# Kernel optimization log

Measured on AMD Instinct MI355X. Metric: run time of the kernel, lower is better.

## Reference

```python
import jax, jax.numpy as jnp
import numpy as np

C = 768        # n_embd
HSZ = 64       # HEAD_SIZE (module-level global in source)
H = C // HSZ   # n_head = 12
G = 2          # conv groups
DL = HSZ       # D_MIX_LORA = HEAD_SIZE
DD = 64        # TIME_DECAY_DIM
DG = C // 4    # D_GATE_LORA
B, T = 2, 2048

PNAMES = ['time_maa_x','time_maa_r','time_maa_w','time_maa_k','time_maa_v','time_maa_a','time_maa_g',
          'time_decay','time_faaaa','time_aaaaa','maa_w1','maa_w2','decay_w1','decay_w2','aaa_w1','aaa_w2',
          'kkk_w1','kkk_w2','gate_w1','gate_w2','w_key','w_value','w_receptance','w_output','ln_x_weight']

def setup_inputs() -> dict:
    key = jax.random.key(0)
    ks = jax.random.split(key, 32)
    f = lambda i, shape, s=1.0: jax.random.normal(ks[i], shape, jnp.float32) * s
    u = lambda i, shape: jax.random.uniform(ks[i], shape, dtype=jnp.float32)
    cs = float(C // G) ** -0.5
    return dict(
        x=f(0, (B, C, T)),
        time_maa_x=u(1, (1, C, 1)), time_maa_r=u(2, (1, C, 1)), time_maa_w=u(3, (1, C, 1)),
        time_maa_k=u(4, (1, C, 1)), time_maa_v=u(5, (1, C, 1)), time_maa_a=u(6, (1, C, 1)),
        time_maa_g=u(7, (1, C, 1)),
        time_decay=f(8, (1, C, 1), 0.5), time_faaaa=f(9, (H, HSZ), 0.1), time_aaaaa=f(10, (1, C, 1), 0.1),
        maa_w1=f(11, (6 * DL, C), 0.02), maa_w2=f(12, (6, DL, C), 0.02),
        decay_w1=f(13, (DD, C), 0.02), decay_w2=f(14, (C, DD), 0.02),
        aaa_w1=f(15, (DD, C), 0.02), aaa_w2=f(16, (C, DD), 0.02),
        kkk_w1=f(17, (DD, C), 0.02), kkk_w2=f(18, (C, DD), 0.02),
        gate_w1=f(19, (DG, C), 0.02), gate_w2=f(20, (C, DG), 0.02),
        w_key=f(21, (G, C // G, C // G), cs), w_value=f(22, (G, C // G, C // G), cs),
        w_receptance=f(23, (G, C // G, C // G), cs), w_output=f(24, (G, C // G, C // G), cs),
        ln_x_weight=jnp.ones((C,), jnp.float32),
    )

def _gconv(x, w):
    # grouped 1x1 Conv1d: x (B,C,T), w (G, C/G out, C/G in) -> (B,C,T)
    b, c, t = x.shape
    xg = x.reshape(b, G, c // G, t)
    return jnp.einsum('goc,bgct->bgot', w, xg).reshape(b, c, t)

def _lora(w1, w2, z):
    # w2 @ tanh(w1 @ z), channels-first z (B,C,T)
    return jnp.einsum('cd,bdt->bct', w2, jnp.tanh(jnp.einsum('dc,bct->bdt', w1, z)))

def _wkv7(r, w, k, v, a, bb):
    # RWKV-7 generalized delta-rule recurrence. All inputs (B,T,C), w in log-decay space.
    b, t, c = r.shape
    rs = lambda x: jnp.moveaxis(x.reshape(b, t, H, HSZ), 1, 0)  # (T,B,H,N)
    r4, k4, v4, a4, b4 = map(rs, (r, k, v, a, bb))
    wdec = rs(jnp.exp(-jnp.exp(w)))
    def step(S, inp):
        rr, ww, kk, vv, aa, b2 = inp  # each (B,H,N)
        sab = jnp.einsum('bhij,bhj,bhk->bhik', S, aa, b2)
        S = S * ww[:, :, None, :] + sab + vv[..., None] * kk[:, :, None, :]
        y = jnp.einsum('bhij,bhj->bhi', S, rr)
        return S, y
    S0 = jnp.zeros((b, H, HSZ, HSZ), r.dtype)
    _, ys = jax.lax.scan(step, S0, (r4, wdec, k4, v4, a4, b4))
    return jnp.moveaxis(ys, 0, 1).reshape(b, t, c)

def _forward(x, time_maa_x, time_maa_r, time_maa_w, time_maa_k, time_maa_v, time_maa_a, time_maa_g,
             time_decay, time_faaaa, time_aaaaa, maa_w1, maa_w2, decay_w1, decay_w2, aaa_w1, aaa_w2,
             kkk_w1, kkk_w2, gate_w1, gate_w2, w_key, w_value, w_receptance, w_output, ln_x_weight):
    b, c, t = x.shape
    xx = x  # shift_mode == 'none'
    xm = x * time_maa_x + xx * (1.0 - time_maa_x)
    tm = jnp.tanh(jnp.einsum('dc,bct->bdt', maa_w1, xm)).reshape(b, 6, DL, t)
    mix = jnp.einsum('bndt,ndc->nbct', tm, maa_w2)  # (6,B,C,T)
    mr, mw, mk, mv, ma, mg = mix
    xr = x + xx * (time_maa_r + mr)
    xw = x + xx * (time_maa_w + mw)
    xk = x + xx * (time_maa_k + mk)
    xv = x + xx * (time_maa_v + mv)
    xa = x + xx * (time_maa_a + ma)
    xg = x + xx * (time_maa_g + mg)
    tr = lambda z: z.transpose(0, 2, 1)  # (B,C,T) -> (B,T,C)
    r = tr(_gconv(xr, w_receptance))
    wlog = tr(-jax.nn.softplus(-(time_decay + _lora(decay_w1, decay_w2, xw))) - 0.5)
    k = tr(_gconv(xk, w_key))
    v = tr(_gconv(xv, w_value))
    g = tr(_lora(gate_w1, gate_w2, xg))
    kk = k + tr(_lora(kkk_w1, kkk_w2, xk))
    kk4 = kk.reshape(b, t, H, HSZ)
    kk = (kk4 / jnp.maximum(jnp.linalg.norm(kk4, axis=-1, keepdims=True), 1e-12)).reshape(b, t, c)
    a = jax.nn.sigmoid(tr(time_aaaaa + _lora(aaa_w1, aaa_w2, xa)))
    y = _wkv7(r, wlog, k, v, -kk, kk * a)
    # ln_x: RMSNorm over channel dim
    y = y * jax.lax.rsqrt(jnp.mean(y * y, axis=-1, keepdims=True) + 1e-5) * ln_x_weight
    rk = (r.reshape(b, t, H, HSZ) * k.reshape(b, t, H, HSZ) * time_faaaa).sum(-1, keepdims=True)
    y = y + (rk * v.reshape(b, t, H, HSZ)).reshape(b, t, c)
    return _gconv(tr(y * g), w_output)  # (B,C,T)

def reference(x, time_maa_x, time_maa_r, time_maa_w, time_maa_k, time_maa_v, time_maa_a, time_maa_g,
              time_decay, time_faaaa, time_aaaaa, maa_w1, maa_w2, decay_w1, decay_w2, aaa_w1, aaa_w2,
              kkk_w1, kkk_w2, gate_w1, gate_w2, w_key, w_value, w_receptance, w_output, ln_x_weight):
    return _forward(x, time_maa_x, time_maa_r, time_maa_w, time_maa_k, time_maa_v, time_maa_a, time_maa_g,
                    time_decay, time_faaaa, time_aaaaa, maa_w1, maa_w2, decay_w1, decay_w2, aaa_w1, aaa_w2,
                    kkk_w1, kkk_w2, gate_w1, gate_w2, w_key, w_value, w_receptance, w_output, ln_x_weight)
```

## Files before the change

### kernel.cpp

```cpp
#include <hip/hip_runtime.h>
#include <math.h>

#define BB 2
#define TT 2048
#define CC 768
#define HH 12
#define NN 64
#define GG 2
#define CG 384
#define FF 3145728L
#define S1 1572864L

typedef __attribute__((ext_vector_type(8))) short bf8frag;
typedef __attribute__((ext_vector_type(4))) float f4acc;

__device__ inline unsigned short f2bf(float x) {
    union { float f; unsigned u; } v; v.f = x;
    unsigned r = v.u + 0x7FFFu + ((v.u >> 16) & 1u);
    return (unsigned short)(r >> 16);
}
__device__ inline float bf2f(unsigned short u) {
    union { unsigned u; float f; } v; v.u = ((unsigned)u) << 16;
    return v.f;
}

template<int ATRANS, int BTRANS, int TOUT, int MODE>
__global__ __launch_bounds__(256) void gemm_kernel(
    const float* __restrict__ A, const float* __restrict__ Bm, float* __restrict__ Cm,
    const float* __restrict__ aux, const float* __restrict__ aux2,
    int K, int ldA, int ldB, int ldC, int zInner,
    long sA_o, long sA_i, long sB_o, long sB_i, long sC_o, long sC_i,
    long sAux_i, long sAux2_o, unsigned short* bfout)
{
    const int zo = blockIdx.z / zInner;
    const int zi = blockIdx.z % zInner;
    A  += (size_t)zo * sA_o + (size_t)zi * sA_i;
    Bm += (size_t)zo * sB_o + (size_t)zi * sB_i;
    Cm += (size_t)zo * sC_o + (size_t)zi * sC_i;
    if (MODE == 2) { aux += (size_t)zi * sAux_i; aux2 += (size_t)zo * sAux2_o; }

    const int m0t = blockIdx.y * 64;
    const int n0t = blockIdx.x * 64;
    const int tid = threadIdx.x;

    __shared__ float As[16][64];
    __shared__ float Bs[16][64];

    int mi, ni;
    if (TOUT) { mi = (tid & 15) * 4; ni = (tid >> 4) * 4; }
    else      { ni = (tid & 15) * 4; mi = (tid >> 4) * 4; }

    float acc[4][4];
#pragma unroll
    for (int i = 0; i < 4; ++i)
#pragma unroll
        for (int j = 0; j < 4; ++j) acc[i][j] = 0.f;

    for (int k0 = 0; k0 < K; k0 += 16) {
        if (!ATRANS) {
            const int row = tid >> 2;
            const int kc  = (tid & 3) * 4;
            float4 av = *(const float4*)&A[(size_t)(m0t + row) * ldA + k0 + kc];
            As[kc + 0][row] = av.x; As[kc + 1][row] = av.y;
            As[kc + 2][row] = av.z; As[kc + 3][row] = av.w;
        } else {
            const int krow = tid >> 4;
            const int mc   = (tid & 15) * 4;
            *(float4*)&As[krow][mc] = *(const float4*)&A[(size_t)(k0 + krow) * ldA + m0t + mc];
        }
        if (!BTRANS) {
            const int krow = tid >> 4;
            const int tc   = (tid & 15) * 4;
            *(float4*)&Bs[krow][tc] = *(const float4*)&Bm[(size_t)(k0 + krow) * ldB + n0t + tc];
        } else {
            const int trow = tid >> 2;
            const int kc   = (tid & 3) * 4;
            float4 bv = *(const float4*)&Bm[(size_t)(n0t + trow) * ldB + k0 + kc];
            Bs[kc + 0][trow] = bv.x; Bs[kc + 1][trow] = bv.y;
            Bs[kc + 2][trow] = bv.z; Bs[kc + 3][trow] = bv.w;
        }
        __syncthreads();
#pragma unroll
        for (int kk = 0; kk < 16; ++kk) {
            float4 a4 = *(const float4*)&As[kk][mi];
            float4 b4 = *(const float4*)&Bs[kk][ni];
            float am[4] = {a4.x, a4.y, a4.z, a4.w};
            float bn[4] = {b4.x, b4.y, b4.z, b4.w};
#pragma unroll
            for (int i = 0; i < 4; ++i)
#pragma unroll
                for (int j = 0; j < 4; ++j) acc[i][j] = fmaf(am[i], bn[j], acc[i][j]);
        }
        __syncthreads();
    }

    const int mbase = m0t + mi, nbase = n0t + ni;
#pragma unroll
    for (int i = 0; i < 4; ++i) {
        float4 xv;
        if (MODE == 2) xv = *(const float4*)&aux2[(size_t)(mbase + i) * ldC + nbase];
        float xa[4] = {0.f, 0.f, 0.f, 0.f};
        if (MODE == 2) { xa[0] = xv.x; xa[1] = xv.y; xa[2] = xv.z; xa[3] = xv.w; }
#pragma unroll
        for (int j = 0; j < 4; ++j) {
            float v = acc[i][j];
            if (MODE == 1) v = tanhf(v);
            else if (MODE == 2) v = xa[j] * (aux[mbase + i] + v);
            else if (MODE == 3) {
                float u  = aux[mbase + i] + v;
                float sp = fmaxf(-u, 0.f) + log1pf(expf(-fabsf(u)));
                float wl = -sp - 0.5f;
                v = expf(-expf(wl));
            } else if (MODE == 4) {
                float u = aux[mbase + i] + v;
                v = 1.f / (1.f + expf(-u));
            }
            acc[i][j] = v;
        }
    }
    if (!TOUT) {
        const bool skipf = (MODE == 2) && (bfout != nullptr) && (zi == 0 || zi == 3);
        if (!skipf) {
#pragma unroll
            for (int i = 0; i < 4; ++i) {
                float4 o = {acc[i][0], acc[i][1], acc[i][2], acc[i][3]};
                *(float4*)&Cm[(size_t)(mbase + i) * ldC + nbase] = o;
            }
        }
        if (MODE == 2 && bfout != nullptr) {
            int sidx = (zi == 0) ? 0 : (zi == 2) ? 1 : (zi == 3) ? 2 : -1;
            if (sidx >= 0) {
                unsigned short* bp = bfout + (size_t)sidx * FF + (size_t)zo * ((long)CC * TT);
#pragma unroll
                for (int i = 0; i < 4; ++i) {
                    ushort4 o = {f2bf(acc[i][0]), f2bf(acc[i][1]), f2bf(acc[i][2]), f2bf(acc[i][3])};
                    *(ushort4*)&bp[(size_t)(mbase + i) * ldC + nbase] = o;
                }
            }
        }
    } else {
#pragma unroll
        for (int j = 0; j < 4; ++j) {
            float4 o = {acc[0][j], acc[1][j], acc[2][j], acc[3][j]};
            *(float4*)&Cm[(size_t)(nbase + j) * ldC + mbase] = o;
        }
    }
}

__global__ __launch_bounds__(256) void lorah_kernel(
    const float* __restrict__ w0, const float* __restrict__ w1,
    const float* __restrict__ w2, const float* __restrict__ w3,
    const float* __restrict__ x0, const float* __restrict__ x1,
    const float* __restrict__ x2, const float* __restrict__ x3,
    float* __restrict__ o0, float* __restrict__ o1,
    float* __restrict__ o2, float* __restrict__ o3)
{
    const int z = blockIdx.z;
    const int which = z >> 1, bz = z & 1;
    if (which < 3 && blockIdx.y > 0) return;
    const float* A; const float* Bm; float* Cm; int M;
    if (which == 0)      { A = w0; Bm = x0; Cm = o0; M = 64; }
    else if (which == 1) { A = w1; Bm = x1; Cm = o1; M = 64; }
    else if (which == 2) { A = w2; Bm = x2; Cm = o2; M = 64; }
    else                 { A = w3; Bm = x3; Cm = o3; M = 192; }
    Bm += (size_t)bz * ((long)CC * TT);
    Cm += (size_t)bz * ((long)M * TT);

    const int m0t = blockIdx.y * 64;
    const int n0t = blockIdx.x * 64;
    const int tid = threadIdx.x;

    __shared__ float As[16][64];
    __shared__ float Bs[16][64];

    const int ni = (tid & 15) * 4, mi = (tid >> 4) * 4;
    float acc[4][4];
#pragma unroll
    for (int i = 0; i < 4; ++i)
#pragma unroll
        for (int j = 0; j < 4; ++j) acc[i][j] = 0.f;

    for (int k0 = 0; k0 < CC; k0 += 16) {
        {
            const int row = tid >> 2, kc = (tid & 3) * 4;
            float4 av = *(const float4*)&A[(size_t)(m0t + row) * CC + k0 + kc];
            As[kc + 0][row] = av.x; As[kc + 1][row] = av.y;
            As[kc + 2][row] = av.z; As[kc + 3][row] = av.w;
        }
        {
            const int krow = tid >> 4, tc = (tid & 15) * 4;
            *(float4*)&Bs[krow][tc] = *(const float4*)&Bm[(size_t)(k0 + krow) * TT + n0t + tc];
        }
        __syncthreads();
#pragma unroll
        for (int kk = 0; kk < 16; ++kk) {
            float4 a4 = *(const float4*)&As[kk][mi];
            float4 b4 = *(const float4*)&Bs[kk][ni];
            float am[4] = {a4.x, a4.y, a4.z, a4.w};
            float bn[4] = {b4.x, b4.y, b4.z, b4.w};
#pragma unroll
            for (int i = 0; i < 4; ++i)
#pragma unroll
                for (int j = 0; j < 4; ++j) acc[i][j] = fmaf(am[i], bn[j], acc[i][j]);
        }
        __syncthreads();
    }
    const int mbase = m0t + mi, nbase = n0t + ni;
#pragma unroll
    for (int i = 0; i < 4; ++i) {
        float4 o = {tanhf(acc[i][0]), tanhf(acc[i][1]), tanhf(acc[i][2]), tanhf(acc[i][3])};
        *(float4*)&Cm[(size_t)(mbase + i) * TT + nbase] = o;
    }
}

__global__ __launch_bounds__(256) void loraout_kernel(
    const float* __restrict__ dw2, const float* __restrict__ aw2,
    const float* __restrict__ kw2,
    const float* __restrict__ dhh, const float* __restrict__ ahh,
    const float* __restrict__ khh,
    const float* __restrict__ tdecay, const float* __restrict__ taaaaa,
    float* __restrict__ wwB, float* __restrict__ b2B, float* __restrict__ aaB)
{
    const int z = blockIdx.z;
    const int which = z >> 1, bz = z & 1;
    const float* A; const float* Bm; float* Cm; const float* aux;
    if (which == 0)      { A = dw2; Bm = dhh; Cm = wwB; aux = tdecay; }
    else if (which == 1) { A = aw2; Bm = ahh; Cm = b2B; aux = taaaaa; }
    else                 { A = kw2; Bm = khh; Cm = aaB; aux = nullptr; }
    Bm += (size_t)bz * (64L * TT);
    Cm += (size_t)bz * ((long)TT * CC);

    const int m0t = blockIdx.y * 64;
    const int n0t = blockIdx.x * 64;
    const int tid = threadIdx.x;

    __shared__ float As[16][64];
    __shared__ float Bs[16][64];

    const int mi = (tid & 15) * 4, ni = (tid >> 4) * 4;
    float acc[4][4];
#pragma unroll
    for (int i = 0; i < 4; ++i)
#pragma unroll
        for (int j = 0; j < 4; ++j) acc[i][j] = 0.f;

    for (int k0 = 0; k0 < 64; k0 += 16) {
        {
            const int row = tid >> 2, kc = (tid & 3) * 4;
            float4 av = *(const float4*)&A[(size_t)(m0t + row) * 64 + k0 + kc];
            As[kc + 0][row] = av.x; As[kc + 1][row] = av.y;
            As[kc + 2][row] = av.z; As[kc + 3][row] = av.w;
        }
        {
            const int krow = tid >> 4, tc = (tid & 15) * 4;
            *(float4*)&Bs[krow][tc] = *(const float4*)&Bm[(size_t)(k0 + krow) * TT + n0t + tc];
        }
        __syncthreads();
#pragma unroll
        for (int kk = 0; kk < 16; ++kk) {
            float4 a4 = *(const float4*)&As[kk][mi];
            float4 b4 = *(const float4*)&Bs[kk][ni];
            float am[4] = {a4.x, a4.y, a4.z, a4.w};
            float bn[4] = {b4.x, b4.y, b4.z, b4.w};
#pragma unroll
            for (int i = 0; i < 4; ++i)
#pragma unroll
                for (int j = 0; j < 4; ++j) acc[i][j] = fmaf(am[i], bn[j], acc[i][j]);
        }
        __syncthreads();
    }
    const int mbase = m0t + mi, nbase = n0t + ni;
#pragma unroll
    for (int i = 0; i < 4; ++i) {
#pragma unroll
        for (int j = 0; j < 4; ++j) {
            float v = acc[i][j];
            if (which == 0) {
                float u  = aux[mbase + i] + v;
                float sp = fmaxf(-u, 0.f) + log1pf(expf(-fabsf(u)));
                v = expf(-expf(-sp - 0.5f));
            } else if (which == 1) {
                float u = aux[mbase + i] + v;
                v = 1.f / (1.f + expf(-u));
            }
            acc[i][j] = v;
        }
    }
#pragma unroll
    for (int j = 0; j < 4; ++j) {
        float4 o = {acc[0][j], acc[1][j], acc[2][j], acc[3][j]};
        *(float4*)&Cm[(size_t)(nbase + j) * CC + mbase] = o;
    }
}

__global__ __launch_bounds__(256) void convs3_mfma_kernel(
    const unsigned short* __restrict__ wball, const unsigned short* __restrict__ X6t,
    float* __restrict__ X6)
{
    const int z = blockIdx.z;
    const int conv = z >> 2, bg = z & 3, b = bg >> 1, g = bg & 1;
    const unsigned short* Wb = wball + (size_t)conv * 294912;
    const unsigned short* Xb = X6t + (size_t)conv * FF;
    const int oslot = (conv == 0) ? 1 : (conv == 1) ? 4 : 5;
    float* Cout = X6 + (size_t)oslot * FF;

    const int t0 = blockIdx.x * 128;
    const int m0 = blockIdx.y * 128;
    const int tid = threadIdx.x;
    const int wave = tid >> 6, lane = tid & 63;
    const int lq = lane >> 4, lr = lane & 15;

    __shared__ unsigned short Ws[128 * 40];
    __shared__ unsigned short Xs[128 * 40];

    const unsigned short* Wg = Wb + (size_t)g * (CG * CG);
    const long xbase = (long)b * (long)TT * CC;

    f4acc acc0[8], acc1[8];
#pragma unroll
    for (int j = 0; j < 8; ++j) { acc0[j] = (f4acc)0.f; acc1[j] = (f4acc)0.f; }

    for (int k0 = 0; k0 < CG; k0 += 32) {
        {
            const int m = tid >> 1, kc = (tid & 1) * 16;
            const unsigned short* src = Wg + (size_t)(m0 + m) * CG + k0 + kc;
            *(bf8frag*)&Ws[m * 40 + kc]     = *(const bf8frag*)src;
            *(bf8frag*)&Ws[m * 40 + kc + 8] = *(const bf8frag*)(src + 8);
        }
        {
            const int t = tid >> 1, kc = (tid & 1) * 16;
            const unsigned short* src = Xb + xbase + (long)(t0 + t) * CC + g * CG + k0 + kc;
            *(bf8frag*)&Xs[t * 40 + kc]     = *(const bf8frag*)src;
            *(bf8frag*)&Xs[t * 40 + kc + 8] = *(const bf8frag*)(src + 8);
        }
        __syncthreads();

        bf8frag a0 = *(const bf8frag*)&Ws[(32 * wave + lr) * 40 + lq * 8];
        bf8frag a1 = *(const bf8frag*)&Ws[(32 * wave + 16 + lr) * 40 + lq * 8];
#pragma unroll
        for (int nj = 0; nj < 8; ++nj) {
            bf8frag bb = *(const bf8frag*)&Xs[(16 * nj + lr) * 40 + lq * 8];
            acc0[nj] = __builtin_amdgcn_mfma_f32_16x16x32_bf16(a0, bb, acc0[nj], 0, 0, 0);
            acc1[nj] = __builtin_amdgcn_mfma_f32_16x16x32_bf16(a1, bb, acc1[nj], 0, 0, 0);
        }
        __syncthreads();
    }

#pragma unroll
    for (int fi = 0; fi < 2; ++fi) {
        const int cbase = m0 + 32 * wave + 16 * fi + lq * 4;
#pragma unroll
        for (int nj = 0; nj < 8; ++nj) {
            const f4acc av = fi ? acc1[nj] : acc0[nj];
            const int t = t0 + 16 * nj + lr;
            float4 o = {av[0], av[1], av[2], av[3]};
            *(float4*)&Cout[(long)b * (long)TT * CC + (long)t * CC + g * CG + cbase] = o;
        }
    }
}

__global__ __launch_bounds__(256) void convout_mfma_kernel(
    const unsigned short* __restrict__ Wb, const unsigned short* __restrict__ Xb,
    float* __restrict__ Cout)
{
    const int bz = blockIdx.z; const int b = bz >> 1, g = bz & 1;
    const int t0 = blockIdx.x * 128;
    const int m0 = blockIdx.y * 128;
    const int tid = threadIdx.x;
    const int wave = tid >> 6, lane = tid & 63;
    const int lq = lane >> 4, lr = lane & 15;

    __shared__ unsigned short Ws[128 * 40];
    __shared__ unsigned short Xs[128 * 40];

    const unsigned short* Wg = Wb + (size_t)g * (CG * CG);
    const long xbase = (long)b * (long)TT * CC;

    f4acc acc0[8], acc1[8];
#pragma unroll
    for (int j = 0; j < 8; ++j) { acc0[j] = (f4acc)0.f; acc1[j] = (f4acc)0.f; }

    for (int k0 = 0; k0 < CG; k0 += 32) {
        {
            const int m = tid >> 1, kc = (tid & 1) * 16;
            const unsigned short* src = Wg + (size_t)(m0 + m) * CG + k0 + kc;
            *(bf8frag*)&Ws[m * 40 + kc]     = *(const bf8frag*)src;
            *(bf8frag*)&Ws[m * 40 + kc + 8] = *(const bf8frag*)(src + 8);
        }
        {
            const int t = tid >> 1, kc = (tid & 1) * 16;
            const unsigned short* src = Xb + xbase + (long)(t0 + t) * CC + g * CG + k0 + kc;
            *(bf8frag*)&Xs[t * 40 + kc]     = *(const bf8frag*)src;
            *(bf8frag*)&Xs[t * 40 + kc + 8] = *(const bf8frag*)(src + 8);
        }
        __syncthreads();

        bf8frag a0 = *(const bf8frag*)&Ws[(32 * wave + lr) * 40 + lq * 8];
        bf8frag a1 = *(const bf8frag*)&Ws[(32 * wave + 16 + lr) * 40 + lq * 8];
#pragma unroll
        for (int nj = 0; nj < 8; ++nj) {
            bf8frag bb = *(const bf8frag*)&Xs[(16 * nj + lr) * 40 + lq * 8];
            acc0[nj] = __builtin_amdgcn_mfma_f32_16x16x32_bf16(a0, bb, acc0[nj], 0, 0, 0);
            acc1[nj] = __builtin_amdgcn_mfma_f32_16x16x32_bf16(a1, bb, acc1[nj], 0, 0, 0);
        }
        __syncthreads();
    }

#pragma unroll
    for (int fi = 0; fi < 2; ++fi) {
        const int cbase = m0 + 32 * wave + 16 * fi + lq * 4;
#pragma unroll
        for (int nj = 0; nj < 8; ++nj) {
            const f4acc av = fi ? acc1[nj] : acc0[nj];
            const int t = t0 + 16 * nj + lr;
#pragma unroll
            for (int i = 0; i < 4; ++i)
                Cout[(long)b * (long)CC * TT + (long)(g * CG + cbase + i) * TT + t] = av[i];
        }
    }
}

__global__ __launch_bounds__(256) void maaw1_mfma_kernel(
    const unsigned short* __restrict__ Wb, const unsigned short* __restrict__ Xb,
    float* __restrict__ Cout)
{
    const int b = blockIdx.z;
    const int t0 = blockIdx.x * 128;
    const int m0 = blockIdx.y * 128;
    const int tid = threadIdx.x;
    const int wave = tid >> 6, lane = tid & 63;
    const int lq = lane >> 4, lr = lane & 15;

    __shared__ unsigned short Ws[128 * 40];
    __shared__ unsigned short Xs[128 * 40];

    const long xbase = (long)b * (long)TT * CC;

    f4acc acc0[8], acc1[8];
#pragma unroll
    for (int j = 0; j < 8; ++j) { acc0[j] = (f4acc)0.f; acc1[j] = (f4acc)0.f; }

    for (int k0 = 0; k0 < CC; k0 += 32) {
        {
            const int m = tid >> 1, kc = (tid & 1) * 16;
            const unsigned short* src = Wb + (size_t)(m0 + m) * CC + k0 + kc;
            *(bf8frag*)&Ws[m * 40 + kc]     = *(const bf8frag*)src;
            *(bf8frag*)&Ws[m * 40 + kc + 8] = *(const bf8frag*)(src + 8);
        }
        {
            const int t = tid >> 1, kc = (tid & 1) * 16;
            const unsigned short* src = Xb + xbase + (long)(t0 + t) * CC + k0 + kc;
            *(bf8frag*)&Xs[t * 40 + kc]     = *(const bf8frag*)src;
            *(bf8frag*)&Xs[t * 40 + kc + 8] = *(const bf8frag*)(src + 8);
        }
        __syncthreads();

        bf8frag a0 = *(const bf8frag*)&Ws[(32 * wave + lr) * 40 + lq * 8];
        bf8frag a1 = *(const bf8frag*)&Ws[(32 * wave + 16 + lr) * 40 + lq * 8];
#pragma unroll
        for (int nj = 0; nj < 8; ++nj) {
            bf8frag bb = *(const bf8frag*)&Xs[(16 * nj + lr) * 40 + lq * 8];
            acc0[nj] = __builtin_amdgcn_mfma_f32_16x16x32_bf16(a0, bb, acc0[nj], 0, 0, 0);
            acc1[nj] = __builtin_amdgcn_mfma_f32_16x16x32_bf16(a1, bb, acc1[nj], 0, 0, 0);
        }
        __syncthreads();
    }

#pragma unroll
    for (int fi = 0; fi < 2; ++fi) {
        const int m = m0 + 32 * wave + 16 * fi + lq * 4;
#pragma unroll
        for (int nj = 0; nj < 8; ++nj) {
            const f4acc av = fi ? acc1[nj] : acc0[nj];
            const int t = t0 + 16 * nj + lr;
#pragma unroll
            for (int i = 0; i < 4; ++i)
                Cout[(long)b * 384 * TT + (long)(m + i) * TT + t] = tanhf(av[i]);
        }
    }
}

__global__ __launch_bounds__(256) void btr_kernel(const unsigned short* __restrict__ xin,
                                                  unsigned short* __restrict__ xout)
{
    __shared__ unsigned short L[64][68];
    const int t0 = blockIdx.x * 64, c0 = blockIdx.y * 64;
    const int s = blockIdx.z >> 1, b = blockIdx.z & 1;
    const int tid = threadIdx.x;
    const int lr = tid >> 4, lc = (tid & 15) * 4;
    const size_t ibase = (size_t)s * FF + (size_t)b * CC * TT;
    const size_t obase = (size_t)s * FF + (size_t)b * TT * CC;
#pragma unroll
    for (int i = 0; i < 4; ++i) {
        int c = lr + i * 16;
        ushort4 v = *(const ushort4*)&xin[ibase + (size_t)(c0 + c) * TT + t0 + lc];
        L[c][lc + 0] = v.x; L[c][lc + 1] = v.y; L[c][lc + 2] = v.z; L[c][lc + 3] = v.w;
    }
    __syncthreads();
#pragma unroll
    for (int i = 0; i < 4; ++i) {
        int t = lr + i * 16;
        ushort4 o = {L[lc + 0][t], L[lc + 1][t], L[lc + 2][t], L[lc + 3][t]};
        *(ushort4*)&xout[obase + (size_t)(t0 + t) * CC + c0 + lc] = o;
    }
}

__global__ __launch_bounds__(256) void wcvt_kernel(
    const float* __restrict__ w0, const float* __restrict__ w1,
    const float* __restrict__ w2, const float* __restrict__ w3,
    const float* __restrict__ w4, unsigned short* __restrict__ wb,
    const float* __restrict__ pr, const float* __restrict__ pw,
    const float* __restrict__ pk, const float* __restrict__ pv,
    const float* __restrict__ pa, const float* __restrict__ pg,
    float* __restrict__ paux,
    const float* __restrict__ xin, unsigned short* __restrict__ xout)
{
    __shared__ unsigned short L[64][68];
    const int bid = blockIdx.x;
    if (bid < 5760) {
        const int i = bid * 256 + threadIdx.x;
        const int which = i / 294912, r = i - which * 294912;
        const float* s = (which == 0) ? w0 : (which == 1) ? w1 : (which == 2) ? w2
                       : (which == 3) ? w3 : w4;
        wb[i] = f2bf(s[r]);
        return;
    }
    if (bid < 6528) {
        const int gb = bid - 5760;
        const int t0 = (gb & 31) * 64;
        const int rest = gb >> 5;
        const int c0 = (rest % 12) * 64;
        const int b  = rest / 12;
        const int tid = threadIdx.x;
        const int lr = tid >> 4, lc = (tid & 15) * 4;
#pragma unroll
        for (int i = 0; i < 4; ++i) {
            int c = lr + i * 16;
            float4 v = *(const float4*)&xin[(size_t)b * CC * TT + (size_t)(c0 + c) * TT + t0 + lc];
            L[c][lc + 0] = f2bf(v.x); L[c][lc + 1] = f2bf(v.y);
            L[c][lc + 2] = f2bf(v.z); L[c][lc + 3] = f2bf(v.w);
        }
        __syncthreads();
#pragma unroll
        for (int i = 0; i < 4; ++i) {
            int t = lr + i * 16;
            ushort4 o = {L[lc + 0][t], L[lc + 1][t], L[lc + 2][t], L[lc + 3][t]};
            *(ushort4*)&xout[(size_t)b * TT * CC + (size_t)(t0 + t) * CC + c0 + lc] = o;
        }
        return;
    }
#pragma unroll
    for (int ch = 0; ch < 3; ++ch) {
        int c = ch * 256 + threadIdx.x;
        paux[0 * CC + c] = 1.f + pr[c];
        paux[1 * CC + c] = 1.f + pw[c];
        paux[2 * CC + c] = 1.f + pk[c];
        paux[3 * CC + c] = 1.f + pv[c];
        paux[4 * CC + c] = 1.f + pa[c];
        paux[5 * CC + c] = 1.f + pg[c];
    }
}

__global__ __launch_bounds__(256) void e1_kernel(const float* __restrict__ kA,
                                                 float* __restrict__ kvecA,
                                                 float* __restrict__ aA)
{
    const size_t base = (size_t)blockIdx.x * CC;
    const int tid = threadIdx.x;
#pragma unroll
    for (int ch = 0; ch < 3; ++ch) {
        int c = ch * 256 + tid;
        float kk = kA[base + c] + kvecA[base + c];
        float ss = kk * kk;
#pragma unroll
        for (int off = 32; off; off >>= 1) ss += __shfl_xor(ss, off, 64);
        float denom = fmaxf(sqrtf(ss), 1e-12f);
        float kkn = kk / denom;
        float av = aA[base + c];
        kvecA[base + c] = -kkn;
        aA[base + c]    = kkn * av;
    }
}

struct WFrag {
    float4 w[2], a[2], b[2], k[2], r[2];
    float vv;
};

__global__ __launch_bounds__(256) void wkv_gate_kernel(
    const float* __restrict__ rA, const float* __restrict__ wA,
    const float* __restrict__ kA, const float* __restrict__ vA,
    const float* __restrict__ aaA, const float* __restrict__ b2A,
    unsigned short* __restrict__ yp8,
    const float* __restrict__ gw2, const float* __restrict__ ghh,
    float* __restrict__ gbuf)
{
    if (blockIdx.x < 192) {
        if (threadIdx.x >= 64) return;
        const int blk = blockIdx.x;
        const int bh = blk % 24, rg = blk / 24;
        const int b = bh / HH, h = bh - b * HH;
        const int lane = threadIdx.x;
        const int jg = lane >> 3, p = lane & 7;
        const int row = rg * 8 + p;
        const int base = b * TT * CC + h * NN;
        const int fo = jg * 8;
        const int ybase = (jg * BB + b) * (TT * CC) + h * NN + row;

        float S[8];
#pragma unroll
        for (int i = 0; i < 8; ++i) S[i] = 0.f;

        WFrag f0, f1, f2;

        auto loadfrag = [&](WFrag& f, int t) {
            const int o = base + t * CC + fo;
#pragma unroll
            for (int q = 0; q < 2; ++q) {
                f.w[q] = *(const float4*)&wA[o + 4 * q];
                f.a[q] = *(const float4*)&aaA[o + 4 * q];
                f.b[q] = *(const float4*)&b2A[o + 4 * q];
                f.k[q] = *(const float4*)&kA[o + 4 * q];
                f.r[q] = *(const float4*)&rA[o + 4 * q];
            }
            f.vv = vA[base + t * CC + row];
        };

        auto stepf = [&](const WFrag& f, int t) {
            const float vv = f.vv;
            float vk[8];
#pragma unroll
            for (int q = 0; q < 2; ++q) {
                vk[4*q+0] = vv * f.k[q].x;
                vk[4*q+1] = vv * f.k[q].y;
                vk[4*q+2] = vv * f.k[q].z;
                vk[4*q+3] = vv * f.k[q].w;
            }

            float t0 = 0.f, t1 = 0.f, t2 = 0.f, t3 = 0.f;
#pragma unroll
            for (int q = 0; q < 2; ++q) {
                float4 a4 = f.a[q];
                t0 = fmaf(S[4*q+0], a4.x, t0);
                t1 = fmaf(S[4*q+1], a4.y, t1);
                t2 = fmaf(S[4*q+2], a4.z, t2);
                t3 = fmaf(S[4*q+3], a4.w, t3);
            }
            float part = (t0 + t1) + (t2 + t3);
            float s08 = __shfl_xor(part,  8, 64);
            float s16 = __shfl_xor(part, 16, 64);
            float s24 = __shfl_xor(part, 24, 64);
            float s32 = __shfl_xor(part, 32, 64);
            float s40 = __shfl_xor(part, 40, 64);
            float s48 = __shfl_xor(part, 48, 64);
            float s56 = __shfl_xor(part, 56, 64);
            float tmp = ((part + s08) + (s16 + s24)) + ((s32 + s40) + (s48 + s56));

            float y0 = 0.f, y1 = 0.f, y2 = 0.f, y3 = 0.f;
#pragma unroll
            for (int q = 0; q < 2; ++q) {
                float4 w4 = f.w[q], b4 = f.b[q], r4 = f.r[q];
                S[4*q+0] = fmaf(S[4*q+0], w4.x, fmaf(tmp, b4.x, vk[4*q+0]));
                y0 = fmaf(S[4*q+0], r4.x, y0);
                S[4*q+1] = fmaf(S[4*q+1], w4.y, fmaf(tmp, b4.y, vk[4*q+1]));
                y1 = fmaf(S[4*q+1], r4.y, y1);
                S[4*q+2] = fmaf(S[4*q+2], w4.z, fmaf(tmp, b4.z, vk[4*q+2]));
                y2 = fmaf(S[4*q+2], r4.z, y2);
                S[4*q+3] = fmaf(S[4*q+3], w4.w, fmaf(tmp, b4.w, vk[4*q+3]));
                y3 = fmaf(S[4*q+3], r4.w, y3);
            }
            yp8[ybase + t * CC] = f2bf((y0 + y1) + (y2 + y3));
        };

        loadfrag(f0, 0);
        loadfrag(f1, 1);
        loadfrag(f2, 2);

        int t = 0;
        for (; t + 2 < TT; t += 3) {
            stepf(f0, t);
            if (t + 3 < TT) loadfrag(f0, t + 3);
            stepf(f1, t + 1);
            if (t + 4 < TT) loadfrag(f1, t + 4);
            stepf(f2, t + 2);
            if (t + 5 < TT) loadfrag(f2, t + 5);
        }
        if (t < TT) stepf(f0, t);
        if (t + 1 < TT) stepf(f1, t + 1);
        return;
    }

    {
        const int gb = blockIdx.x - 192;
        const int n0t = (gb & 31) * 64;
        const int rest = gb >> 5;
        const int m0t = (rest % 12) * 64;
        const int bz  = rest / 12;
        const float* A  = gw2;
        const float* Bm = ghh + (size_t)bz * (192L * TT);
        float* Cm = gbuf + (size_t)bz * ((long)TT * CC);
        const int tid = threadIdx.x;

        __shared__ float As[16][64];
        __shared__ float Bs[16][64];

        const int mi = (tid & 15) * 4, ni = (tid >> 4) * 4;
        float acc[4][4];
#pragma unroll
        for (int i = 0; i < 4; ++i)
#pragma unroll
            for (int j = 0; j < 4; ++j) acc[i][j] = 0.f;

        for (int k0 = 0; k0 < 192; k0 += 16) {
            {
                const int row = tid >> 2, kc = (tid & 3) * 4;
                float4 av = *(const float4*)&A[(size_t)(m0t + row) * 192 + k0 + kc];
                As[kc + 0][row] = av.x; As[kc + 1][row] = av.y;
                As[kc + 2][row] = av.z; As[kc + 3][row] = av.w;
            }
            {
                const int krow = tid >> 4, tc = (tid & 15) * 4;
                *(float4*)&Bs[krow][tc] = *(const float4*)&Bm[(size_t)(k0 + krow) * TT + n0t + tc];
            }
            __syncthreads();
#pragma unroll
            for (int kk = 0; kk < 16; ++kk) {
                float4 a4 = *(const float4*)&As[kk][mi];
                float4 b4 = *(const float4*)&Bs[kk][ni];
                float am[4] = {a4.x, a4.y, a4.z, a4.w};
                float bn[4] = {b4.x, b4.y, b4.z, b4.w};
#pragma unroll
                for (int i = 0; i < 4; ++i)
#pragma unroll
                    for (int j = 0; j < 4; ++j) acc[i][j] = fmaf(am[i], bn[j], acc[i][j]);
            }
            __syncthreads();
        }
        const int mbase = m0t + mi, nbase = n0t + ni;
#pragma unroll
        for (int j = 0; j < 4; ++j) {
            float4 o = {acc[0][j], acc[1][j], acc[2][j], acc[3][j]};
            *(float4*)&Cm[(size_t)(nbase + j) * CC + mbase] = o;
        }
    }
}

__global__ __launch_bounds__(256) void e2_kernel(
    const unsigned short* __restrict__ yp8, const float* __restrict__ rA,
    const float* __restrict__ kA, const float* __restrict__ vA,
    const float* __restrict__ gA, const float* __restrict__ faaaa,
    const float* __restrict__ lnw, unsigned short* __restrict__ zB)
{
    const int bt = blockIdx.x;
    const int b = bt / TT, t = bt - b * TT;
    const size_t base = (size_t)bt * CC;
    const int tid = threadIdx.x;
    const int wave = tid >> 6;
    __shared__ float red[4];
    __shared__ float rk[12];

    float yv[3];
    float ss = 0.f;
#pragma unroll
    for (int ch = 0; ch < 3; ++ch) {
        int c = ch * 256 + tid;
        float y = 0.f;
#pragma unroll
        for (int jg = 0; jg < 8; ++jg)
            y += bf2f(yp8[((size_t)(jg * BB + b) * TT + t) * CC + c]);
        yv[ch] = y;
        ss = fmaf(y, y, ss);
        float p = rA[base + c] * kA[base + c] * faaaa[c];
#pragma unroll
        for (int off = 32; off; off >>= 1) p += __shfl_xor(p, off, 64);
        if ((tid & 63) == 0) rk[ch * 4 + wave] = p;
    }
#pragma unroll
    for (int off = 32; off; off >>= 1) ss += __shfl_xor(ss, off, 64);
    if ((tid & 63) == 0) red[wave] = ss;
    __syncthreads();
    const float total = red[0] + red[1] + red[2] + red[3];
    const float scale = rsqrtf(total / (float)CC + 1e-5f);
#pragma unroll
    for (int ch = 0; ch < 3; ++ch) {
        int c = ch * 256 + tid;
        float out = yv[ch] * scale * lnw[c] + rk[c >> 6] * vA[base + c];
        zB[base + c] = f2bf(out * gA[base + c]);
    }
}

extern "C" void kernel_launch(void* const* d_in, const int* in_sizes, int n_in,
                              void* d_out, int out_size, void* d_ws, size_t ws_size,
                              hipStream_t stream)
{
    (void)in_sizes; (void)n_in; (void)out_size; (void)ws_size;
    const float* x        = (const float*)d_in[0];
    const float* tmaa_r   = (const float*)d_in[2];
    const float* tmaa_w   = (const float*)d_in[3];
    const float* tmaa_k   = (const float*)d_in[4];
    const float* tmaa_v   = (const float*)d_in[5];
    const float* tmaa_a   = (const float*)d_in[6];
    const float* tmaa_g   = (const float*)d_in[7];
    const float* tdecay   = (const float*)d_in[8];
    const float* tfaaaa   = (const float*)d_in[9];
    const float* taaaaa   = (const float*)d_in[10];
    const float* maa_w1   = (const float*)d_in[11];
    const float* maa_w2   = (const float*)d_in[12];
    const float* decay_w1 = (const float*)d_in[13];
    const float* decay_w2 = (const float*)d_in[14];
    const float* aaa_w1   = (const float*)d_in[15];
    const float* aaa_w2   = (const float*)d_in[16];
    const float* kkk_w1   = (const float*)d_in[17];
    const float* kkk_w2   = (const float*)d_in[18];
    const float* gate_w1  = (const float*)d_in[19];
    const float* gate_w2  = (const float*)d_in[20];
    const float* w_key    = (const float*)d_in[21];
    const float* w_value  = (const float*)d_in[22];
    const float* w_recept = (const float*)d_in[23];
    const float* w_output = (const float*)d_in[24];
    const float* lnw      = (const float*)d_in[25];
    float* out = (float*)d_out;

    float* ws   = (float*)d_ws;
    float* paux = ws;
    float* tm   = ws + 8192;
    float* X6   = tm + S1;
    float* dh   = X6 + 6 * FF;
    float* ah   = dh + 262144;
    float* kh   = ah + 262144;
    float* gh   = kh + 262144;
    float* gbuf = gh + 786432;
    unsigned short* yp8 = (unsigned short*)(gbuf + FF);
    unsigned short* X6b = yp8 + 8 * FF;
    unsigned short* zb  = X6b + 3 * FF;
    unsigned short* wb  = zb + FF;
    unsigned short* xtb = wb + 5L * 294912;
    unsigned short* X6t = xtb + FF;

    float* xw = X6 + 1 * FF; float* xk = X6 + 2 * FF;
    float* xa = X6 + 4 * FF; float* xg = X6 + 5 * FF;
    float* wwB = X6 + 0 * FF; float* rB  = X6 + 1 * FF; float* aaB = X6 + 2 * FF;
    float* b2B = X6 + 3 * FF; float* kB  = X6 + 4 * FF; float* vB  = X6 + 5 * FF;

    const long CT = (long)CC * TT;
    const long TC = (long)TT * CC;

    wcvt_kernel<<<dim3(6529), 256, 0, stream>>>(
        w_recept, w_key, w_value, w_output, maa_w1, wb,
        tmaa_r, tmaa_w, tmaa_k, tmaa_v, tmaa_a, tmaa_g, paux,
        x, xtb);

    maaw1_mfma_kernel<<<dim3(16, 3, 2), 256, 0, stream>>>(wb + 4L * 294912, xtb, tm);

    gemm_kernel<1,0,0,2><<<dim3(32, 12, 12), 256, 0, stream>>>(
        maa_w2, tm, X6, paux, x,
        64, 768, TT, TT, 6,
        0, 64L * 768, 384L * TT, 64L * TT, CT, FF, 768, CT, X6b);

    btr_kernel<<<dim3(32, 12, 6), 256, 0, stream>>>(X6b, X6t);

    lorah_kernel<<<dim3(32, 3, 8), 256, 0, stream>>>(
        decay_w1, aaa_w1, kkk_w1, gate_w1, xw, xa, xk, xg, dh, ah, kh, gh);

    convs3_mfma_kernel<<<dim3(16, 3, 12), 256, 0, stream>>>(wb, X6t, X6);

    loraout_kernel<<<dim3(32, 12, 6), 256, 0, stream>>>(
        decay_w2, aaa_w2, kkk_w2, dh, ah, kh, tdecay, taaaaa, wwB, b2B, aaB);

    e1_kernel<<<dim3(BB * TT), 256, 0, stream>>>(kB, aaB, b2B);

    wkv_gate_kernel<<<dim3(960), 256, 0, stream>>>(
        rB, wwB, kB, vB, aaB, b2B, yp8, gate_w2, gh, gbuf);

    e2_kernel<<<dim3(BB * TT), 256, 0, stream>>>(yp8, rB, kB, vB, gbuf, tfaaaa, lnw, zb);

    convout_mfma_kernel<<<dim3(16, 3, 4), 256, 0, stream>>>(wb + 3L * 294912, zb, out);
}
```

Baseline: 768.0 us.

## Merge independent lora, transpose and conv kernels into two combined launches

```diff
diff --git a/kernel.cpp b/kernel.cpp
--- a/kernel.cpp
+++ b/kernel.cpp
@@ -147,163 +147,268 @@
     }
 }
 
-__global__ __launch_bounds__(256) void lorah_kernel(
-    const float* __restrict__ w0, const float* __restrict__ w1,
-    const float* __restrict__ w2, const float* __restrict__ w3,
-    const float* __restrict__ x0, const float* __restrict__ x1,
-    const float* __restrict__ x2, const float* __restrict__ x3,
-    float* __restrict__ o0, float* __restrict__ o1,
-    float* __restrict__ o2, float* __restrict__ o3)
-{
-    const int z = blockIdx.z;
-    const int which = z >> 1, bz = z & 1;
-    if (which < 3 && blockIdx.y > 0) return;
-    const float* A; const float* Bm; float* Cm; int M;
-    if (which == 0)      { A = w0; Bm = x0; Cm = o0; M = 64; }
-    else if (which == 1) { A = w1; Bm = x1; Cm = o1; M = 64; }
-    else if (which == 2) { A = w2; Bm = x2; Cm = o2; M = 64; }
-    else                 { A = w3; Bm = x3; Cm = o3; M = 192; }
-    Bm += (size_t)bz * ((long)CC * TT);
-    Cm += (size_t)bz * ((long)M * TT);
-
-    const int m0t = blockIdx.y * 64;
-    const int n0t = blockIdx.x * 64;
+__global__ __launch_bounds__(256) void prep2_kernel(
+    const float* __restrict__ dw1, const float* __restrict__ aw1,
+    const float* __restrict__ kw1, const float* __restrict__ gw1,
+    const float* __restrict__ xw, const float* __restrict__ xa,
+    const float* __restrict__ xk, const float* __restrict__ xg,
+    float* __restrict__ dh, float* __restrict__ ah,
+    float* __restrict__ kh, float* __restrict__ gh,
+    const unsigned short* __restrict__ X6b, unsigned short* __restrict__ X6t)
+{
+    __shared__ __align__(16) unsigned char smem[8704];
+    const int lb = blockIdx.x;
     const int tid = threadIdx.x;
 
-    __shared__ float As[16][64];
-    __shared__ float Bs[16][64];
-
-    const int ni = (tid & 15) * 4, mi = (tid >> 4) * 4;
-    float acc[4][4];
-#pragma unroll
-    for (int i = 0; i < 4; ++i)
-#pragma unroll
-        for (int j = 0; j < 4; ++j) acc[i][j] = 0.f;
-
-    for (int k0 = 0; k0 < CC; k0 += 16) {
-        {
-            const int row = tid >> 2, kc = (tid & 3) * 4;
-            float4 av = *(const float4*)&A[(size_t)(m0t + row) * CC + k0 + kc];
-            As[kc + 0][row] = av.x; As[kc + 1][row] = av.y;
-            As[kc + 2][row] = av.z; As[kc + 3][row] = av.w;
-        }
-        {
-            const int krow = tid >> 4, tc = (tid & 15) * 4;
-            *(float4*)&Bs[krow][tc] = *(const float4*)&Bm[(size_t)(k0 + krow) * TT + n0t + tc];
+    if (lb < 384) {
+        const float* A; const float* Bm; float* Cm;
+        int m0t, n0t, bz, M;
+        if (lb < 192) {
+            const int xt = lb & 31, rest = lb >> 5;
+            m0t = (rest % 3) * 64; bz = rest / 3;
+            n0t = xt * 64; M = 192;
+            A = gw1; Bm = xg; Cm = gh;
+        } else {
+            const int sb = lb - 192;
+            const int which = sb >> 6, r = sb & 63;
+            const int xt = r & 31; bz = r >> 5;
+            m0t = 0; n0t = xt * 64; M = 64;
+            A  = which == 0 ? dw1 : which == 1 ? aw1 : kw1;
+            Bm = which == 0 ? xw  : which == 1 ? xa  : xk;
+            Cm = which == 0 ? dh  : which == 1 ? ah  : kh;
+        }
+        Bm += (size_t)bz * ((long)CC * TT);
+        Cm += (size_t)bz * ((long)M * TT);
+
+        float (*As)[64] = (float (*)[64])smem;
+        float (*Bs)[64] = (float (*)[64])(smem + 4096);
+
+        const int ni = (tid & 15) * 4, mi = (tid >> 4) * 4;
+        float acc[4][4];
+#pragma unroll
+        for (int i = 0; i < 4; ++i)
+#pragma unroll
+            for (int j = 0; j < 4; ++j) acc[i][j] = 0.f;
+
+        for (int k0 = 0; k0 < CC; k0 += 16) {
+            {
+                const int row = tid >> 2, kc = (tid & 3) * 4;
+                float4 av = *(const float4*)&A[(size_t)(m0t + row) * CC + k0 + kc];
+                As[kc + 0][row] = av.x; As[kc + 1][row] = av.y;
+                As[kc + 2][row] = av.z; As[kc + 3][row] = av.w;
+            }
+            {
+                const int krow = tid >> 4, tc = (tid & 15) * 4;
+                *(float4*)&Bs[krow][tc] = *(const float4*)&Bm[(size_t)(k0 + krow) * TT + n0t + tc];
+            }
+            __syncthreads();
+#pragma unroll
+            for (int kk = 0; kk < 16; ++kk) {
+                float4 a4 = *(const float4*)&As[kk][mi];
+                float4 b4 = *(const float4*)&Bs[kk][ni];
+                float am[4] = {a4.x, a4.y, a4.z, a4.w};
+                float bn[4] = {b4.x, b4.y, b4.z, b4.w};
+#pragma unroll
+                for (int i = 0; i < 4; ++i)
+#pragma unroll
+                    for (int j = 0; j < 4; ++j) acc[i][j] = fmaf(am[i], bn[j], acc[i][j]);
+            }
+            __syncthreads();
+        }
+        const int mbase = m0t + mi, nbase = n0t + ni;
+#pragma unroll
+        for (int i = 0; i < 4; ++i) {
+            float4 o = {tanhf(acc[i][0]), tanhf(acc[i][1]), tanhf(acc[i][2]), tanhf(acc[i][3])};
+            *(float4*)&Cm[(size_t)(mbase + i) * TT + nbase] = o;
+        }
+        return;
+    }
+
+    {
+        const int tb = lb - 384;
+        const int t0 = (tb & 31) * 64;
+        const int rest = tb >> 5;
+        const int c0 = (rest % 12) * 64;
+        const int zc = rest / 12;
+        const int s = zc >> 1, b = zc & 1;
+        unsigned short (*L)[68] = (unsigned short (*)[68])smem;
+        const int lr = tid >> 4, lc = (tid & 15) * 4;
+        const size_t ibase = (size_t)s * FF + (size_t)b * CC * TT;
+        const size_t obase = (size_t)s * FF + (size_t)b * TT * CC;
+#pragma unroll
+        for (int i = 0; i < 4; ++i) {
+            int c = lr + i * 16;
+            ushort4 v = *(const ushort4*)&X6b[ibase + (size_t)(c0 + c) * TT + t0 + lc];
+            L[c][lc + 0] = v.x; L[c][lc + 1] = v.y; L[c][lc + 2] = v.z; L[c][lc + 3] = v.w;
         }
         __syncthreads();
 #pragma unroll
-        for (int kk = 0; kk < 16; ++kk) {
-            float4 a4 = *(const float4*)&As[kk][mi];
-            float4 b4 = *(const float4*)&Bs[kk][ni];
-            float am[4] = {a4.x, a4.y, a4.z, a4.w};
-            float bn[4] = {b4.x, b4.y, b4.z, b4.w};
-#pragma unroll
-            for (int i = 0; i < 4; ++i)
-#pragma unroll
-                for (int j = 0; j < 4; ++j) acc[i][j] = fmaf(am[i], bn[j], acc[i][j]);
-        }
-        __syncthreads();
-    }
-    const int mbase = m0t + mi, nbase = n0t + ni;
-#pragma unroll
-    for (int i = 0; i < 4; ++i) {
-        float4 o = {tanhf(acc[i][0]), tanhf(acc[i][1]), tanhf(acc[i][2]), tanhf(acc[i][3])};
-        *(float4*)&Cm[(size_t)(mbase + i) * TT + nbase] = o;
-    }
-}
-
-__global__ __launch_bounds__(256) void loraout_kernel(
+        for (int i = 0; i < 4; ++i) {
+            int t = lr + i * 16;
+            ushort4 o = {L[lc + 0][t], L[lc + 1][t], L[lc + 2][t], L[lc + 3][t]};
+            *(ushort4*)&X6t[obase + (size_t)(t0 + t) * CC + c0 + lc] = o;
+        }
+    }
+}
+
+__global__ __launch_bounds__(256) void mid2_kernel(
     const float* __restrict__ dw2, const float* __restrict__ aw2,
     const float* __restrict__ kw2,
     const float* __restrict__ dhh, const float* __restrict__ ahh,
     const float* __restrict__ khh,
     const float* __restrict__ tdecay, const float* __restrict__ taaaaa,
-    float* __restrict__ wwB, float* __restrict__ b2B, float* __restrict__ aaB)
-{
-    const int z = blockIdx.z;
-    const int which = z >> 1, bz = z & 1;
-    const float* A; const float* Bm; float* Cm; const float* aux;
-    if (which == 0)      { A = dw2; Bm = dhh; Cm = wwB; aux = tdecay; }
-    else if (which == 1) { A = aw2; Bm = ahh; Cm = b2B; aux = taaaaa; }
-    else                 { A = kw2; Bm = khh; Cm = aaB; aux = nullptr; }
-    Bm += (size_t)bz * (64L * TT);
-    Cm += (size_t)bz * ((long)TT * CC);
-
-    const int m0t = blockIdx.y * 64;
-    const int n0t = blockIdx.x * 64;
-    const int tid = threadIdx.x;
-
-    __shared__ float As[16][64];
-    __shared__ float Bs[16][64];
-
-    const int mi = (tid & 15) * 4, ni = (tid >> 4) * 4;
-    float acc[4][4];
-#pragma unroll
-    for (int i = 0; i < 4; ++i)
-#pragma unroll
-        for (int j = 0; j < 4; ++j) acc[i][j] = 0.f;
-
-    for (int k0 = 0; k0 < 64; k0 += 16) {
-        {
-            const int row = tid >> 2, kc = (tid & 3) * 4;
-            float4 av = *(const float4*)&A[(size_t)(m0t + row) * 64 + k0 + kc];
-            As[kc + 0][row] = av.x; As[kc + 1][row] = av.y;
-            As[kc + 2][row] = av.z; As[kc + 3][row] = av.w;
-        }
-        {
-            const int krow = tid >> 4, tc = (tid & 15) * 4;
-            *(float4*)&Bs[krow][tc] = *(const float4*)&Bm[(size_t)(k0 + krow) * TT + n0t + tc];
-        }
-        __syncthreads();
-#pragma unroll
-        for (int kk = 0; kk < 16; ++kk) {
-            float4 a4 = *(const float4*)&As[kk][mi];
-            float4 b4 = *(const float4*)&Bs[kk][ni];
-            float am[4] = {a4.x, a4.y, a4.z, a4.w};
-            float bn[4] = {b4.x, b4.y, b4.z, b4.w};
-#pragma unroll
-            for (int i = 0; i < 4; ++i)
-#pragma unroll
-                for (int j = 0; j < 4; ++j) acc[i][j] = fmaf(am[i], bn[j], acc[i][j]);
-        }
-        __syncthreads();
-    }
-    const int mbase = m0t + mi, nbase = n0t + ni;
-#pragma unroll
-    for (int i = 0; i < 4; ++i) {
-#pragma unroll
-        for (int j = 0; j < 4; ++j) {
-            float v = acc[i][j];
-            if (which == 0) {
-                float u  = aux[mbase + i] + v;
-                float sp = fmaxf(-u, 0.f) + log1pf(expf(-fabsf(u)));
-                v = expf(-expf(-sp - 0.5f));
-            } else if (which == 1) {
-                float u = aux[mbase + i] + v;
-                v = 1.f / (1.f + expf(-u));
-            }
-            acc[i][j] = v;
-        }
-    }
-#pragma unroll
-    for (int j = 0; j < 4; ++j) {
-        float4 o = {acc[0][j], acc[1][j], acc[2][j], acc[3][j]};
-        *(float4*)&Cm[(size_t)(nbase + j) * CC + mbase] = o;
-    }
-}
-
-__global__ __launch_bounds__(256) void convs3_mfma_kernel(
+    float* __restrict__ wwB, float* __restrict__ b2B, float* __restrict__ aaB,
     const unsigned short* __restrict__ wball, const unsigned short* __restrict__ X6t,
     float* __restrict__ X6)
 {
-    const int z = blockIdx.z;
-    const int conv = z >> 2, bg = z & 3, b = bg >> 1, g = bg & 1;
-    const unsigned short* Wb = wball + (size_t)conv * 294912;
-    const unsigned short* Xb = X6t + (size_t)conv * FF;
-    const int oslot = (conv == 0) ? 1 : (conv == 1) ? 4 : 5;
-    float* Cout = X6 + (size_t)oslot * FF;
-
+    __shared__ __align__(16) unsigned char smem[20480];
+    const int lb = blockIdx.x;
+    const int tid = threadIdx.x;
+
+    if (lb < 2304) {
+        const int xt = lb & 31, rest = lb >> 5;
+        const int yt = rest % 12, z = rest / 12;
+        const int which = z >> 1, bz = z & 1;
+        const float* A; const float* Bm; float* Cm; const float* aux;
+        if (which == 0)      { A = dw2; Bm = dhh; Cm = wwB; aux = tdecay; }
+        else if (which == 1) { A = aw2; Bm = ahh; Cm = b2B; aux = taaaaa; }
+        else                 { A = kw2; Bm = khh; Cm = aaB; aux = nullptr; }
+        Bm += (size_t)bz * (64L * TT);
+        Cm += (size_t)bz * ((long)TT * CC);
+
+        const int m0t = yt * 64;
+        const int n0t = xt * 64;
+
+        float (*As)[64] = (float (*)[64])smem;
+        float (*Bs)[64] = (float (*)[64])(smem + 4096);
+
+        const int mi = (tid & 15) * 4, ni = (tid >> 4) * 4;
+        float acc[4][4];
+#pragma unroll
+        for (int i = 0; i < 4; ++i)
+#pragma unroll
+            for (int j = 0; j < 4; ++j) acc[i][j] = 0.f;
+
+        for (int k0 = 0; k0 < 64; k0 += 16) {
+            {
+                const int row = tid >> 2, kc = (tid & 3) * 4;
+                float4 av = *(const float4*)&A[(size_t)(m0t + row) * 64 + k0 + kc];
+                As[kc + 0][row] = av.x; As[kc + 1][row] = av.y;
+                As[kc + 2][row] = av.z; As[kc + 3][row] = av.w;
+            }
+            {
+                const int krow = tid >> 4, tc = (tid & 15) * 4;
+                *(float4*)&Bs[krow][tc] = *(const float4*)&Bm[(size_t)(k0 + krow) * TT + n0t + tc];
+            }
+            __syncthreads();
+#pragma unroll
+            for (int kk = 0; kk < 16; ++kk) {
+                float4 a4 = *(const float4*)&As[kk][mi];
+                float4 b4 = *(const float4*)&Bs[kk][ni];
+                float am[4] = {a4.x, a4.y, a4.z, a4.w};
+                float bn[4] = {b4.x, b4.y, b4.z, b4.w};
+#pragma unroll
+                for (int i = 0; i < 4; ++i)
+#pragma unroll
+                    for (int j = 0; j < 4; ++j) acc[i][j] = fmaf(am[i], bn[j], acc[i][j]);
+            }
+            __syncthreads();
+        }
+        const int mbase = m0t + mi, nbase = n0t + ni;
+#pragma unroll
+        for (int i = 0; i < 4; ++i) {
+#pragma unroll
+            for (int j = 0; j < 4; ++j) {
+                float v = acc[i][j];
+                if (which == 0) {
+                    float u  = aux[mbase + i] + v;
+                    float sp = fmaxf(-u, 0.f) + log1pf(expf(-fabsf(u)));
+                    v = expf(-expf(-sp - 0.5f));
+                } else if (which == 1) {
+                    float u = aux[mbase + i] + v;
+                    v = 1.f / (1.f + expf(-u));
+                }
+                acc[i][j] = v;
+            }
+        }
+#pragma unroll
+        for (int j = 0; j < 4; ++j) {
+            float4 o = {acc[0][j], acc[1][j], acc[2][j], acc[3][j]};
+            *(float4*)&Cm[(size_t)(nbase + j) * CC + mbase] = o;
+        }
+        return;
+    }
+
+    {
+        const int cb = lb - 2304;
+        const int xt = cb & 15, rest = cb >> 4;
+        const int yt = rest % 3, z = rest / 3;
+        const int conv = z >> 2, bg = z & 3, b = bg >> 1, g = bg & 1;
+        const unsigned short* Wb = wball + (size_t)conv * 294912;
+        const unsigned short* Xb = X6t + (size_t)conv * FF;
+        const int oslot = (conv == 0) ? 1 : (conv == 1) ? 4 : 5;
+        float* Cout = X6 + (size_t)oslot * FF;
+
+        const int t0 = xt * 128;
+        const int m0 = yt * 128;
+        const int wave = tid >> 6, lane = tid & 63;
+        const int lq = lane >> 4, lr = lane & 15;
+
+        unsigned short* Ws = (unsigned short*)smem;
+        unsigned short* Xs = (unsigned short*)(smem + 10240);
+
+        const unsigned short* Wg = Wb + (size_t)g * (CG * CG);
+        const long xbase = (long)b * (long)TT * CC;
+
+        f4acc acc0[8], acc1[8];
+#pragma unroll
+        for (int j = 0; j < 8; ++j) { acc0[j] = (f4acc)0.f; acc1[j] = (f4acc)0.f; }
+
+        for (int k0 = 0; k0 < CG; k0 += 32) {
+            {
+                const int m = tid >> 1, kc = (tid & 1) * 16;
+                const unsigned short* src = Wg + (size_t)(m0 + m) * CG + k0 + kc;
+                *(bf8frag*)&Ws[m * 40 + kc]     = *(const bf8frag*)src;
+                *(bf8frag*)&Ws[m * 40 + kc + 8] = *(const bf8frag*)(src + 8);
+            }
+            {
+                const int t = tid >> 1, kc = (tid & 1) * 16;
+                const unsigned short* src = Xb + xbase + (long)(t0 + t) * CC + g * CG + k0 + kc;
+                *(bf8frag*)&Xs[t * 40 + kc]     = *(const bf8frag*)src;
+                *(bf8frag*)&Xs[t * 40 + kc + 8] = *(const bf8frag*)(src + 8);
+            }
+            __syncthreads();
+
+            bf8frag a0 = *(const bf8frag*)&Ws[(32 * wave + lr) * 40 + lq * 8];
+            bf8frag a1 = *(const bf8frag*)&Ws[(32 * wave + 16 + lr) * 40 + lq * 8];
+#pragma unroll
+            for (int nj = 0; nj < 8; ++nj) {
+                bf8frag bb = *(const bf8frag*)&Xs[(16 * nj + lr) * 40 + lq * 8];
+                acc0[nj] = __builtin_amdgcn_mfma_f32_16x16x32_bf16(a0, bb, acc0[nj], 0, 0, 0);
+                acc1[nj] = __builtin_amdgcn_mfma_f32_16x16x32_bf16(a1, bb, acc1[nj], 0, 0, 0);
+            }
+            __syncthreads();
+        }
+
+#pragma unroll
+        for (int fi = 0; fi < 2; ++fi) {
+            const int cbase = m0 + 32 * wave + 16 * fi + lq * 4;
+#pragma unroll
+            for (int nj = 0; nj < 8; ++nj) {
+                const f4acc av = fi ? acc1[nj] : acc0[nj];
+                const int t = t0 + 16 * nj + lr;
+                float4 o = {av[0], av[1], av[2], av[3]};
+                *(float4*)&Cout[(long)b * (long)TT * CC + (long)t * CC + g * CG + cbase] = o;
+            }
+        }
+    }
+}
+
+__global__ __launch_bounds__(256) void convout_mfma_kernel(
+    const unsigned short* __restrict__ Wb, const unsigned short* __restrict__ Xb,
+    float* __restrict__ Cout)
+{
+    const int bz = blockIdx.z; const int b = bz >> 1, g = bz & 1;
     const int t0 = blockIdx.x * 128;
     const int m0 = blockIdx.y * 128;
     const int tid = threadIdx.x;
@@ -353,66 +458,6 @@
         for (int nj = 0; nj < 8; ++nj) {
             const f4acc av = fi ? acc1[nj] : acc0[nj];
             const int t = t0 + 16 * nj + lr;
-            float4 o = {av[0], av[1], av[2], av[3]};
-            *(float4*)&Cout[(long)b * (long)TT * CC + (long)t * CC + g * CG + cbase] = o;
-        }
-    }
-}
-
-__global__ __launch_bounds__(256) void convout_mfma_kernel(
-    const unsigned short* __restrict__ Wb, const unsigned short* __restrict__ Xb,
-    float* __restrict__ Cout)
-{
-    const int bz = blockIdx.z; const int b = bz >> 1, g = bz & 1;
-    const int t0 = blockIdx.x * 128;
-    const int m0 = blockIdx.y * 128;
-    const int tid = threadIdx.x;
-    const int wave = tid >> 6, lane = tid & 63;
-    const int lq = lane >> 4, lr = lane & 15;
-
-    __shared__ unsigned short Ws[128 * 40];
-    __shared__ unsigned short Xs[128 * 40];
-
-    const unsigned short* Wg = Wb + (size_t)g * (CG * CG);
-    const long xbase = (long)b * (long)TT * CC;
-
-    f4acc acc0[8], acc1[8];
-#pragma unroll
-    for (int j = 0; j < 8; ++j) { acc0[j] = (f4acc)0.f; acc1[j] = (f4acc)0.f; }
-
-    for (int k0 = 0; k0 < CG; k0 += 32) {
-        {
-            const int m = tid >> 1, kc = (tid & 1) * 16;
-            const unsigned short* src = Wg + (size_t)(m0 + m) * CG + k0 + kc;
-            *(bf8frag*)&Ws[m * 40 + kc]     = *(const bf8frag*)src;
-            *(bf8frag*)&Ws[m * 40 + kc + 8] = *(const bf8frag*)(src + 8);
-        }
-        {
-            const int t = tid >> 1, kc = (tid & 1) * 16;
-            const unsigned short* src = Xb + xbase + (long)(t0 + t) * CC + g * CG + k0 + kc;
-            *(bf8frag*)&Xs[t * 40 + kc]     = *(const bf8frag*)src;
-            *(bf8frag*)&Xs[t * 40 + kc + 8] = *(const bf8frag*)(src + 8);
-        }
-        __syncthreads();
-
-        bf8frag a0 = *(const bf8frag*)&Ws[(32 * wave + lr) * 40 + lq * 8];
-        bf8frag a1 = *(const bf8frag*)&Ws[(32 * wave + 16 + lr) * 40 + lq * 8];
-#pragma unroll
-        for (int nj = 0; nj < 8; ++nj) {
-            bf8frag bb = *(const bf8frag*)&Xs[(16 * nj + lr) * 40 + lq * 8];
-            acc0[nj] = __builtin_amdgcn_mfma_f32_16x16x32_bf16(a0, bb, acc0[nj], 0, 0, 0);
-            acc1[nj] = __builtin_amdgcn_mfma_f32_16x16x32_bf16(a1, bb, acc1[nj], 0, 0, 0);
-        }
-        __syncthreads();
-    }
-
-#pragma unroll
-    for (int fi = 0; fi < 2; ++fi) {
-        const int cbase = m0 + 32 * wave + 16 * fi + lq * 4;
-#pragma unroll
-        for (int nj = 0; nj < 8; ++nj) {
-            const f4acc av = fi ? acc1[nj] : acc0[nj];
-            const int t = t0 + 16 * nj + lr;
 #pragma unroll
             for (int i = 0; i < 4; ++i)
                 Cout[(long)b * (long)CC * TT + (long)(g * CG + cbase + i) * TT + t] = av[i];
@@ -477,31 +522,6 @@
             for (int i = 0; i < 4; ++i)
                 Cout[(long)b * 384 * TT + (long)(m + i) * TT + t] = tanhf(av[i]);
         }
-    }
-}
-
-__global__ __launch_bounds__(256) void btr_kernel(const unsigned short* __restrict__ xin,
-                                                  unsigned short* __restrict__ xout)
-{
-    __shared__ unsigned short L[64][68];
-    const int t0 = blockIdx.x * 64, c0 = blockIdx.y * 64;
-    const int s = blockIdx.z >> 1, b = blockIdx.z & 1;
-    const int tid = threadIdx.x;
-    const int lr = tid >> 4, lc = (tid & 15) * 4;
-    const size_t ibase = (size_t)s * FF + (size_t)b * CC * TT;
-    const size_t obase = (size_t)s * FF + (size_t)b * TT * CC;
-#pragma unroll
-    for (int i = 0; i < 4; ++i) {
-        int c = lr + i * 16;
-        ushort4 v = *(const ushort4*)&xin[ibase + (size_t)(c0 + c) * TT + t0 + lc];
-        L[c][lc + 0] = v.x; L[c][lc + 1] = v.y; L[c][lc + 2] = v.z; L[c][lc + 3] = v.w;
-    }
-    __syncthreads();
-#pragma unroll
-    for (int i = 0; i < 4; ++i) {
-        int t = lr + i * 16;
-        ushort4 o = {L[lc + 0][t], L[lc + 1][t], L[lc + 2][t], L[lc + 3][t]};
-        *(ushort4*)&xout[obase + (size_t)(t0 + t) * CC + c0 + lc] = o;
     }
 }
 
@@ -857,15 +877,13 @@
         64, 768, TT, TT, 6,
         0, 64L * 768, 384L * TT, 64L * TT, CT, FF, 768, CT, X6b);
 
-    btr_kernel<<<dim3(32, 12, 6), 256, 0, stream>>>(X6b, X6t);
-
-    lorah_kernel<<<dim3(32, 3, 8), 256, 0, stream>>>(
-        decay_w1, aaa_w1, kkk_w1, gate_w1, xw, xa, xk, xg, dh, ah, kh, gh);
-
-    convs3_mfma_kernel<<<dim3(16, 3, 12), 256, 0, stream>>>(wb, X6t, X6);
-
-    loraout_kernel<<<dim3(32, 12, 6), 256, 0, stream>>>(
-        decay_w2, aaa_w2, kkk_w2, dh, ah, kh, tdecay, taaaaa, wwB, b2B, aaB);
+    prep2_kernel<<<dim3(2688), 256, 0, stream>>>(
+        decay_w1, aaa_w1, kkk_w1, gate_w1, xw, xa, xk, xg,
+        dh, ah, kh, gh, X6b, X6t);
+
+    mid2_kernel<<<dim3(2880), 256, 0, stream>>>(
+        decay_w2, aaa_w2, kkk_w2, dh, ah, kh, tdecay, taaaaa,
+        wwB, b2B, aaB, wb, X6t, X6);
 
     e1_kernel<<<dim3(BB * TT), 256, 0, stream>>>(kB, aaB, b2B);
 
```

New measurement: 777.7 us. About the same (+1.3%).
